# Performance work log

Hardware: AMD Instinct MI355X
Metric: run time of the kernel (lower is better)

## Reference

```python
import jax, jax.numpy as jnp
import numpy as np

T = 4096          # timesteps per modality
D_QK = 64
D = D_QK + 2      # feature dim incl. timestamp channel = 66
M = 4             # number of modalities
N_LIN = 3         # n_layers=2 hidden layers -> 3 Linear layers in the MLP


def setup_inputs() -> dict:
    key = jax.random.key(0)
    ks = jax.random.split(key, 2 * M + 2)
    inp = {}
    for m in range(M):
        feats = jax.random.normal(ks[2 * m], (1, 1, T, D - 1), dtype=jnp.float32)
        # last feature channel is a sorted event timestamp, as the source reads X[0,0,:,-1]
        ts = jnp.sort(jax.random.uniform(ks[2 * m + 1], (T,), dtype=jnp.float32))
        inp[f"x{m + 1}"] = jnp.concatenate([feats, ts[None, None, :, None]], axis=-1)
    scale = 1.0 / np.sqrt(D).astype(np.float32)
    inp["wq"] = jax.random.normal(ks[2 * M], (N_LIN, D, D), dtype=jnp.float32) * scale
    inp["bq"] = jnp.zeros((N_LIN, D), dtype=jnp.float32)
    inp["wk"] = jax.random.normal(ks[2 * M + 1], (N_LIN, D, D), dtype=jnp.float32) * scale
    inp["bk"] = jnp.zeros((N_LIN, D), dtype=jnp.float32)
    return inp


def _mlp(x, W, b):
    # MLP(d, [d]*2, d, relu): relu after hidden linears, none after the last
    h = x
    for i in range(N_LIN - 1):
        h = jax.nn.relu(h @ W[i] + b[i])
    return h @ W[N_LIN - 1] + b[N_LIN - 1]


def _causal_dot_product(Q, K, V, t1, t2):
    """Cross-modality causal linear attention with timestamps.
    Q:(T1,d) queries at times t1; K:(T2,d), V:(T2,dv) at times t2 (sorted).
    out[i] = Q[i] @ sum_{j : t2[j] <= t1[i]} K[j] (x) V[j]
    Implemented as a cumulative outer-product state + gather (scan form).
    """
    state = jnp.cumsum(K[:, :, None] * V[:, None, :], axis=0)   # (T2, d, dv)
    idx = jnp.searchsorted(t2, t1, side="right") - 1            # last key with t2 <= t1[i]
    S = state[jnp.clip(idx, 0)]                                  # (T1, d, dv)
    S = jnp.where((idx >= 0)[:, None, None], S, jnp.zeros_like(S))
    return jnp.einsum("td,tdv->tv", Q, S)                        # (T1, dv)


def reference(x1, x2, x3, x4, wq, bq, wk, bk):
    xs = [x1, x2, x3, x4]
    Q = _mlp(x1, wq, bq)[0, 0]      # (T1, D)
    t1 = x1[0, 0, :, -1]
    outs = []
    for xm in xs:                   # fixed small loop over M modalities
        Km = _mlp(xm, wk, bk)[0, 0]  # shared W_K[0], as in the source
        Vm = xm[0, 0]                # V = X
        t2 = xm[0, 0, :, -1]
        outs.append(_causal_dot_product(Q, Km, Vm, t1, t2))
    Z = jnp.stack(outs, axis=0)     # (M, T1, D) == Zout[0]
    yhat = Z.sum(0)[None, :, :2]    # (1, T1, 2)
    return yhat
```

## Files before the change

kernel.cpp:

```cpp
#include <hip/hip_runtime.h>

#define T 4096
#define D 66
#define NL 3
#define NC 64
#define JC 64
#define DD (D * D)
#define HSB 104
#define KTS 68

typedef short bf16x8 __attribute__((ext_vector_type(8)));
typedef float f32x4  __attribute__((ext_vector_type(4)));

__device__ __forceinline__ short f2bf(float f) {
    unsigned int u = __builtin_bit_cast(unsigned int, f);
    u += 0x7fff + ((u >> 16) & 1);
    return (short)(u >> 16);
}

__global__ __launch_bounds__(256) void mlp_scan_kernel(
    const float* __restrict__ x1, const float* __restrict__ x2,
    const float* __restrict__ x3, const float* __restrict__ x4,
    const float* __restrict__ wq, const float* __restrict__ bq,
    const float* __restrict__ wk, const float* __restrict__ bk,
    float* __restrict__ Q, float* __restrict__ S,
    float* __restrict__ chunkSum, float* __restrict__ TM)
{
    __shared__ short Hs[64 * HSB];
    __shared__ short Wt[80 * HSB];
    __shared__ float KT[D * KTS];
    __shared__ float side[3][64];

    const int t    = threadIdx.x;
    const bool isQ = blockIdx.x >= 256;
    const int m    = isQ ? 0 : (blockIdx.x >> 6);
    const int j0   = (isQ ? (blockIdx.x - 256) : (blockIdx.x & 63)) * 64;
    const float* X  = (isQ || m == 0) ? x1 : (m == 1 ? x2 : (m == 2 ? x3 : x4));
    const float* W  = isQ ? wq : wk;
    const float* Bs = isQ ? bq : bk;

    const float* xt = X + (size_t)j0 * D;
    for (int k = t; k < 64 * D; k += 256) {
        const int r = k / D;
        const int d = k - r * D;
        const float v = xt[k];
        Hs[r * HSB + d] = f2bf(v);
        if (d < 2) side[d][r] = v;
        if (d == D - 1) side[2][r] = v;
    }
    for (int k = t; k < 64 * (HSB - D); k += 256) {
        const int r = k / (HSB - D);
        const int d = D + (k - r * (HSB - D));
        Hs[r * HSB + d] = 0;
    }
    {
        int* wz = (int*)Wt;
        for (int k = t; k < 80 * HSB / 2; k += 256) wz[k] = 0;
    }

    float wreg[18];
#pragma unroll
    for (int i = 0; i < 18; ++i) {
        const int k = t + i * 256;
        if (k < DD) wreg[i] = W[k];
    }

    const int lane = t & 63;
    const int wv   = t >> 6;
    const int lrow = lane & 15;
    const int kg   = (lane >> 4) * 8;
    const int cr0  = (lane >> 4) * 4;

    __syncthreads();

#pragma unroll 1
    for (int l = 0; l < NL; ++l) {
#pragma unroll
        for (int i = 0; i < 18; ++i) {
            const int k = t + i * 256;
            if (k < DD) {
                const int kk = k / D;
                const int o  = k - kk * D;
                Wt[o * HSB + kk] = f2bf(wreg[i]);
            }
        }
        __syncthreads();

        if (l < NL - 1) {
            const float* Wg = W + (l + 1) * DD;
#pragma unroll
            for (int i = 0; i < 18; ++i) {
                const int k = t + i * 256;
                if (k < DD) wreg[i] = Wg[k];
            }
        }

        const int abase = (wv * 16 + lrow) * HSB + kg;
        const bf16x8 a0 = *(const bf16x8*)&Hs[abase];
        const bf16x8 a1 = *(const bf16x8*)&Hs[abase + 32];
        const bf16x8 a2 = *(const bf16x8*)&Hs[abase + 64];

        f32x4 acc[5];
#pragma unroll
        for (int nt = 0; nt < 5; ++nt) {
            const short* wb = &Wt[(nt * 16 + lrow) * HSB + kg];
            f32x4 c = {0.0f, 0.0f, 0.0f, 0.0f};
            c = __builtin_amdgcn_mfma_f32_16x16x32_bf16(a0, *(const bf16x8*)(wb),      c, 0, 0, 0);
            c = __builtin_amdgcn_mfma_f32_16x16x32_bf16(a1, *(const bf16x8*)(wb + 32), c, 0, 0, 0);
            c = __builtin_amdgcn_mfma_f32_16x16x32_bf16(a2, *(const bf16x8*)(wb + 64), c, 0, 0, 0);
            acc[nt] = c;
        }
        __syncthreads();

#pragma unroll
        for (int nt = 0; nt < 5; ++nt) {
            const int col = nt * 16 + lrow;
            const float bias = (col < D) ? Bs[l * D + col] : 0.0f;
#pragma unroll
            for (int r = 0; r < 4; ++r) {
                const int row = wv * 16 + cr0 + r;
                float v = acc[nt][r] + bias;
                if (l < NL - 1) {
                    v = fmaxf(v, 0.0f);
                    Hs[row * HSB + col] = f2bf(v);
                } else if (isQ) {
                    if (col < D) Q[(size_t)(j0 + row) * D + col] = v;
                } else {
                    if (col < D) KT[col * KTS + row] = v;
                }
            }
        }
    }

    __syncthreads();

    if (!isQ) {
        const int c = t;
        if (c >= 144 && c < 144 + JC) TM[m * T + j0 + (c - 144)] = side[2][c - 144];
        if (c < 132) {
            const int d = c >> 1;
            const int v = c & 1;
            float run = 0.0f;
#pragma unroll 8
            for (int jj = 0; jj < JC; ++jj) {
                run = fmaf(KT[d * KTS + jj], side[v][jj], run);
                S[((size_t)m * T + j0 + jj) * 132 + c] = run;
            }
            chunkSum[((size_t)m * NC + j0 / JC) * 132 + c] = run;
        }
    }
}

__global__ __launch_bounds__(256) void chunkscan_kernel(
    const float* __restrict__ chunkSum, float* __restrict__ chunkOff)
{
    const int wv   = threadIdx.x >> 6;
    const int lane = threadIdx.x & 63;
    const int c    = blockIdx.x * 4 + wv;
    const int m    = blockIdx.y;
    if (c >= 132) return;

    const float v = chunkSum[((size_t)m * NC + lane) * 132 + c];
    float inc = v;
#pragma unroll
    for (int off = 1; off < 64; off <<= 1) {
        const float y = __shfl_up(inc, off);
        if (lane >= off) inc += y;
    }
    chunkOff[((size_t)m * NC + lane) * 132 + c] = inc - v;
}

__global__ __launch_bounds__(256) void out_kernel(
    const float* __restrict__ Q, const float* __restrict__ S,
    const float* __restrict__ chunkOff, const float* __restrict__ TM,
    float* __restrict__ out)
{
    __shared__ float segEnd[4][64];
    const int w    = threadIdx.x >> 6;
    const int lane = threadIdx.x & 63;
    const int i    = blockIdx.x * 4 + w;

    segEnd[w][lane] = TM[w * T + lane * 64 + 63];
    const float t1i = TM[i];
    const float q0  = Q[(size_t)i * D + lane];
    const float q1  = (lane < 2) ? Q[(size_t)i * D + 64 + lane] : 0.0f;
    float acc0 = 0.0f, acc1 = 0.0f;
    __syncthreads();

    int seg[4];
#pragma unroll
    for (int mm = 0; mm < 4; ++mm) {
        const unsigned long long b = __ballot(segEnd[mm][lane] <= t1i);
        const int hi = __popcll(b);
        seg[mm] = (hi < 63) ? hi : 63;
    }
    int idx[4];
#pragma unroll
    for (int mm = 0; mm < 4; ++mm) {
        const float sv = TM[mm * T + seg[mm] * 64 + lane];
        const unsigned long long b = __ballot(sv <= t1i);
        idx[mm] = seg[mm] * 64 + __popcll(b) - 1;
    }

#pragma unroll
    for (int mm = 0; mm < 4; ++mm) {
        if (idx[mm] >= 0) {
            const float* sp = S + ((size_t)mm * T + idx[mm]) * 132;
            const float* op = chunkOff + ((size_t)mm * NC + (idx[mm] / JC)) * 132;
            const float2 s0 = *(const float2*)(sp + lane * 2);
            const float2 c0 = *(const float2*)(op + lane * 2);
            acc0 = fmaf(q0, s0.x + c0.x, acc0);
            acc1 = fmaf(q0, s0.y + c0.y, acc1);
            if (lane < 2) {
                const float2 s1 = *(const float2*)(sp + 128 + lane * 2);
                const float2 c1 = *(const float2*)(op + 128 + lane * 2);
                acc0 = fmaf(q1, s1.x + c1.x, acc0);
                acc1 = fmaf(q1, s1.y + c1.y, acc1);
            }
        }
    }

#pragma unroll
    for (int off = 32; off >= 1; off >>= 1) {
        acc0 += __shfl_down(acc0, off);
        acc1 += __shfl_down(acc1, off);
    }
    if (lane == 0) {
        out[(size_t)i * 2 + 0] = acc0;
        out[(size_t)i * 2 + 1] = acc1;
    }
}

extern "C" void kernel_launch(void* const* d_in, const int* in_sizes, int n_in,
                              void* d_out, int out_size, void* d_ws, size_t ws_size,
                              hipStream_t stream)
{
    (void)in_sizes; (void)n_in; (void)out_size; (void)ws_size;
    const float* x1 = (const float*)d_in[0];
    const float* x2 = (const float*)d_in[1];
    const float* x3 = (const float*)d_in[2];
    const float* x4 = (const float*)d_in[3];
    const float* wq = (const float*)d_in[4];
    const float* bq = (const float*)d_in[5];
    const float* wk = (const float*)d_in[6];
    const float* bk = (const float*)d_in[7];

    float* ws = (float*)d_ws;
    float* Q        = ws;
    float* S        = ws + 270336;
    float* chunkSum = ws + 2433024;
    float* chunkOff = ws + 2466816;
    float* TM       = ws + 2500608;

    mlp_scan_kernel<<<320, 256, 0, stream>>>(x1, x2, x3, x4, wq, bq, wk, bk,
                                             Q, S, chunkSum, TM);
    chunkscan_kernel<<<dim3(33, 4), 256, 0, stream>>>(chunkSum, chunkOff);
    out_kernel<<<1024, 256, 0, stream>>>(Q, S, chunkOff, TM, (float*)d_out);
}
```

Measured before the change: 29.51 us.

## Fuse chunk-offset scan into MLP kernel via last-block atomic counter

Removes the separate chunkscan kernel launch. Each K block writes its chunk sum with cache-bypassing stores and bumps a per-modality atomic counter, and the last block to finish scans all 64 chunk sums for that modality. The input load is also changed to use float2 reads. This saves one launch and its gap, but adds a memset launch, a serialized tail scan done by a single block per modality, and reliance on correct memory ordering through sc0/sc1 loads and stores with relaxed atomics.

New measurement: 43.07 us. 45.9% more time.

```diff
diff --git a/kernel.cpp b/kernel.cpp
--- a/kernel.cpp
+++ b/kernel.cpp
@@ -18,18 +18,24 @@
     return (short)(u >> 16);
 }
 
+__device__ __forceinline__ void st_sc(float* p, float v) {
+    asm volatile("global_store_dword %0, %1, off sc0 sc1" :: "v"(p), "v"(v));
+}
+
 __global__ __launch_bounds__(256) void mlp_scan_kernel(
     const float* __restrict__ x1, const float* __restrict__ x2,
     const float* __restrict__ x3, const float* __restrict__ x4,
     const float* __restrict__ wq, const float* __restrict__ bq,
     const float* __restrict__ wk, const float* __restrict__ bk,
     float* __restrict__ Q, float* __restrict__ S,
-    float* __restrict__ chunkSum, float* __restrict__ TM)
+    float* __restrict__ chunkSum, float* __restrict__ chunkOff,
+    float* __restrict__ TM, int* __restrict__ done)
 {
     __shared__ short Hs[64 * HSB];
     __shared__ short Wt[80 * HSB];
     __shared__ float KT[D * KTS];
     __shared__ float side[3][64];
+    __shared__ int lastFlag;
 
     const int t    = threadIdx.x;
     const bool isQ = blockIdx.x >= 256;
@@ -39,14 +45,15 @@
     const float* W  = isQ ? wq : wk;
     const float* Bs = isQ ? bq : bk;
 
-    const float* xt = X + (size_t)j0 * D;
-    for (int k = t; k < 64 * D; k += 256) {
-        const int r = k / D;
-        const int d = k - r * D;
-        const float v = xt[k];
-        Hs[r * HSB + d] = f2bf(v);
-        if (d < 2) side[d][r] = v;
-        if (d == D - 1) side[2][r] = v;
+    const float2* xt2 = (const float2*)(X + (size_t)j0 * D);
+    for (int k = t; k < 64 * 33; k += 256) {
+        const int r  = k / 33;
+        const int dp = (k - r * 33) * 2;
+        const float2 v = xt2[k];
+        Hs[r * HSB + dp]     = f2bf(v.x);
+        Hs[r * HSB + dp + 1] = f2bf(v.y);
+        if (dp == 0)  { side[0][r] = v.x; side[1][r] = v.y; }
+        if (dp == 64) { side[2][r] = v.y; }
     }
     for (int k = t; k < 64 * (HSB - D); k += 256) {
         const int r = k / (HSB - D);
@@ -132,9 +139,11 @@
         }
     }
 
-    __syncthreads();
-
-    if (!isQ) {
+    if (isQ) return;
+
+    __syncthreads();
+
+    {
         const int c = t;
         if (c >= 144 && c < 144 + JC) TM[m * T + j0 + (c - 144)] = side[2][c - 144];
         if (c < 132) {
@@ -146,28 +155,70 @@
                 run = fmaf(KT[d * KTS + jj], side[v][jj], run);
                 S[((size_t)m * T + j0 + jj) * 132 + c] = run;
             }
-            chunkSum[((size_t)m * NC + j0 / JC) * 132 + c] = run;
-        }
-    }
-}
-
-__global__ __launch_bounds__(256) void chunkscan_kernel(
-    const float* __restrict__ chunkSum, float* __restrict__ chunkOff)
-{
-    const int wv   = threadIdx.x >> 6;
-    const int lane = threadIdx.x & 63;
-    const int c    = blockIdx.x * 4 + wv;
-    const int m    = blockIdx.y;
-    if (c >= 132) return;
-
-    const float v = chunkSum[((size_t)m * NC + lane) * 132 + c];
-    float inc = v;
-#pragma unroll
-    for (int off = 1; off < 64; off <<= 1) {
-        const float y = __shfl_up(inc, off);
-        if (lane >= off) inc += y;
-    }
-    chunkOff[((size_t)m * NC + lane) * 132 + c] = inc - v;
+            st_sc(chunkSum + ((size_t)m * NC + j0 / JC) * 132 + c, run);
+        }
+    }
+
+    asm volatile("s_waitcnt vmcnt(0)" ::: "memory");
+    __syncthreads();
+    if (t == 0) {
+        const int old = __hip_atomic_fetch_add(&done[m], 1, __ATOMIC_RELAXED,
+                                               __HIP_MEMORY_SCOPE_AGENT);
+        lastFlag = (old == NC - 1);
+    }
+    __syncthreads();
+    if (!lastFlag) return;
+
+    {
+        const float* base = chunkSum + ((size_t)m * NC + lane) * 132;
+#pragma unroll 1
+        for (int g = 0; g < 32; g += 8) {
+            const float *p0 = base + (wv + 4 * (g + 0)), *p1 = base + (wv + 4 * (g + 1));
+            const float *p2 = base + (wv + 4 * (g + 2)), *p3 = base + (wv + 4 * (g + 3));
+            const float *p4 = base + (wv + 4 * (g + 4)), *p5 = base + (wv + 4 * (g + 5));
+            const float *p6 = base + (wv + 4 * (g + 6)), *p7 = base + (wv + 4 * (g + 7));
+            float a0, a1, a2, a3, a4, a5, a6, a7;
+            asm volatile(
+                "global_load_dword %0, %8, off sc0 sc1\n\t"
+                "global_load_dword %1, %9, off sc0 sc1\n\t"
+                "global_load_dword %2, %10, off sc0 sc1\n\t"
+                "global_load_dword %3, %11, off sc0 sc1\n\t"
+                "global_load_dword %4, %12, off sc0 sc1\n\t"
+                "global_load_dword %5, %13, off sc0 sc1\n\t"
+                "global_load_dword %6, %14, off sc0 sc1\n\t"
+                "global_load_dword %7, %15, off sc0 sc1\n\t"
+                "s_waitcnt vmcnt(0)"
+                : "=&v"(a0), "=&v"(a1), "=&v"(a2), "=&v"(a3),
+                  "=&v"(a4), "=&v"(a5), "=&v"(a6), "=&v"(a7)
+                : "v"(p0), "v"(p1), "v"(p2), "v"(p3),
+                  "v"(p4), "v"(p5), "v"(p6), "v"(p7));
+            float va[8] = {a0, a1, a2, a3, a4, a5, a6, a7};
+#pragma unroll
+            for (int i = 0; i < 8; ++i) {
+                float inc = va[i];
+#pragma unroll
+                for (int off = 1; off < 64; off <<= 1) {
+                    const float y = __shfl_up(inc, off);
+                    if (lane >= off) inc += y;
+                }
+                chunkOff[((size_t)m * NC + lane) * 132 + (wv + 4 * (g + i))] = inc - va[i];
+            }
+        }
+        {
+            float vv;
+            const float* pr = base + (wv + 128);
+            asm volatile("global_load_dword %0, %1, off sc0 sc1\n\t"
+                         "s_waitcnt vmcnt(0)"
+                         : "=&v"(vv) : "v"(pr));
+            float inc = vv;
+#pragma unroll
+            for (int off = 1; off < 64; off <<= 1) {
+                const float y = __shfl_up(inc, off);
+                if (lane >= off) inc += y;
+            }
+            chunkOff[((size_t)m * NC + lane) * 132 + (wv + 128)] = inc - vv;
+        }
+    }
 }
 
 __global__ __launch_bounds__(256) void out_kernel(
@@ -251,9 +302,11 @@
     float* chunkSum = ws + 2433024;
     float* chunkOff = ws + 2466816;
     float* TM       = ws + 2500608;
+    int*   done     = (int*)(ws + 2516992);
+
+    hipMemsetAsync(done, 0, 4 * sizeof(int), stream);
 
     mlp_scan_kernel<<<320, 256, 0, stream>>>(x1, x2, x3, x4, wq, bq, wk, bk,
-                                             Q, S, chunkSum, TM);
-    chunkscan_kernel<<<dim3(33, 4), 256, 0, stream>>>(chunkSum, chunkOff);
+                                             Q, S, chunkSum, chunkOff, TM, done);
     out_kernel<<<1024, 256, 0, stream>>>(Q, S, chunkOff, TM, (float*)d_out);
 }
```
